# Performance work log

Measured on AMD Instinct MI355X. Metric: run time of the kernel, lower is better.

## Reference

```python
import jax, jax.numpy as jnp
import numpy as np

VOCAB, HID, KS, VS, EMB = 30, 512, 128, 128, 256
T, N, MAXLEN = 1000, 256, 250

def _lstm_cell(x, h, c, w_ih, w_hh, b_ih, b_hh):
    gates = x @ w_ih.T + h @ w_hh.T + b_ih + b_hh
    i, f, g, o = jnp.split(gates, 4, axis=-1)
    c2 = jax.nn.sigmoid(f) * c + jax.nn.sigmoid(i) * jnp.tanh(g)
    h2 = jax.nn.sigmoid(o) * jnp.tanh(c2)
    return h2, c2

def setup_inputs() -> dict:
    key = jax.random.key(0)
    ks = jax.random.split(key, 20)
    p = lambda k, shp: (jax.random.normal(k, shp, dtype=jnp.float32) * 0.05)
    inp = {
        'keys': jax.random.normal(ks[0], (T, N, KS), dtype=jnp.float32),
        'values': jax.random.normal(ks[1], (T, N, VS), dtype=jnp.float32),
        'seq_lengths': jax.random.randint(ks[2], (N,), 1, T + 1),
        'text': jax.random.randint(ks[3], (N, MAXLEN), 0, VOCAB),
        'embed_W': p(ks[4], (VOCAB, EMB)),
        'w_ih1': p(ks[5], (4 * HID, EMB + VS)), 'w_hh1': p(ks[6], (4 * HID, HID)),
        'b_ih1': jnp.zeros((4 * HID,), jnp.float32), 'b_hh1': jnp.zeros((4 * HID,), jnp.float32),
        'w_ih2': p(ks[7], (4 * HID, HID)), 'w_hh2': p(ks[8], (4 * HID, HID)),
        'b_ih2': jnp.zeros((4 * HID,), jnp.float32), 'b_hh2': jnp.zeros((4 * HID,), jnp.float32),
        'w_ih3': p(ks[9], (4 * KS, HID)), 'w_hh3': p(ks[10], (4 * KS, KS)),
        'b_ih3': jnp.zeros((4 * KS,), jnp.float32), 'b_hh3': jnp.zeros((4 * KS,), jnp.float32),
        'lin_W': p(ks[11], (KS, KS + VS)), 'lin_b': jnp.zeros((KS,), jnp.float32),
        'char_W': p(ks[12], (VOCAB, KS)), 'char_b': jnp.zeros((VOCAB,), jnp.float32),
    }
    return inp

def reference(keys, values, seq_lengths, text, embed_W,
              w_ih1, w_hh1, b_ih1, b_hh1,
              w_ih2, w_hh2, b_ih2, b_hh2,
              w_ih3, w_hh3, b_ih3, b_hh3,
              lin_W, lin_b, char_W, char_b):
    # teacher forcing path (deterministic), dropout is identity in reference
    mask = jnp.arange(T)[None, :] >= seq_lengths[:, None]          # (N, T)
    embs = embed_W[text]                                           # (N, MAXLEN, EMB)
    embs = jnp.swapaxes(embs, 0, 1)                                # (MAXLEN, N, EMB)

    def step(carry, emb_t):
        h1, c1, h2, c2, h3, c3, ctx = carry
        inp1 = jnp.concatenate([emb_t, ctx], axis=1)
        h1, c1 = _lstm_cell(inp1, h1, c1, w_ih1, w_hh1, b_ih1, b_hh1)
        h2, c2 = _lstm_cell(h1, h2, c2, w_ih2, w_hh2, b_ih2, b_hh2)
        h3, c3 = _lstm_cell(h2, h3, c3, w_ih3, w_hh3, b_ih3, b_hh3)
        energy = jnp.einsum('tnk,nk->nt', keys, h3)                # (N, T)
        energy = jnp.where(mask, -1e9, energy)
        attn = jax.nn.softmax(energy, axis=1)
        ctx2 = jnp.einsum('nt,tnv->nv', attn, values)              # (N, VS)
        pred = jnp.concatenate([h3, ctx2], axis=1) @ lin_W.T + lin_b
        pred = pred @ char_W.T + char_b                            # (N, VOCAB)
        return (h1, c1, h2, c2, h3, c3, ctx2), (pred, attn)

    z = lambda d: jnp.zeros((N, d), jnp.float32)
    init = (z(HID), z(HID), z(HID), z(HID), z(KS), z(KS), values[-1])
    _, (preds, attns) = jax.lax.scan(step, init, embs)
    return jnp.swapaxes(preds, 0, 1), attns                        # (N, MAXLEN, VOCAB), (MAXLEN, N, T)
```

## Files before the change

### kernel.cpp

```cpp
#include <hip/hip_runtime.h>

#define VOCAB  30
#define HID    512
#define KS     128
#define VS     128
#define EMB    256
#define TT     1000
#define NB     256
#define MAXLEN 250

#define NH (NB*HID)
#define NK (NB*KS)
#define OFF_CTX (6*NH + 3*NK)
#define WS_TOTAL (OFF_CTX + NK)
#define STATE_BYTES ((size_t)WS_TOTAL * 4)
#define VBF_BYTES   ((size_t)TT * NB * VS * 2)

#define K1 (EMB + VS + HID)
#define K2 (HID + HID)
#define K3 (HID + KS)
#define W1SZ (4*HID*K1)
#define W2SZ (4*HID*K2)
#define W3SZ (4*KS*K3)
#define EMBSZ (VOCAB*EMB)
#define BS1 (4*HID)
#define BS2 (4*HID)
#define BS3 (4*KS)

constexpr size_t NEW_BASE  = STATE_BYTES + VBF_BYTES;
constexpr size_t OFF_W1HI  = NEW_BASE;
constexpr size_t OFF_W1LO  = OFF_W1HI + (size_t)W1SZ*2;
constexpr size_t OFF_W2HI  = OFF_W1LO + (size_t)W1SZ*2;
constexpr size_t OFF_W2LO  = OFF_W2HI + (size_t)W2SZ*2;
constexpr size_t OFF_W3HI  = OFF_W2LO + (size_t)W2SZ*2;
constexpr size_t OFF_W3LO  = OFF_W3HI + (size_t)W3SZ*2;
constexpr size_t OFF_EMBHI = OFF_W3LO + (size_t)W3SZ*2;
constexpr size_t OFF_EMBLO = OFF_EMBHI + (size_t)EMBSZ*2;
constexpr size_t OFF_BSUM  = OFF_EMBLO + (size_t)EMBSZ*2;
constexpr size_t OFF_CTXHI = OFF_BSUM  + (size_t)(BS1+BS2+BS3)*4;
constexpr size_t OFF_CTXLO = OFF_CTXHI + (size_t)NB*VS*2;
constexpr size_t OFF_H1HI  = OFF_CTXLO + (size_t)NB*VS*2;
constexpr size_t OFF_H1LO  = OFF_H1HI + (size_t)2*NH*2;
constexpr size_t OFF_H2HI  = OFF_H1LO + (size_t)2*NH*2;
constexpr size_t OFF_H2LO  = OFF_H2HI + (size_t)2*NH*2;
constexpr size_t OFF_H3HI  = OFF_H2LO + (size_t)2*NH*2;
constexpr size_t OFF_H3LO  = OFF_H3HI + (size_t)2*NK*2;
constexpr size_t OFF_H3F   = OFF_H3LO + (size_t)2*NK*2;
constexpr size_t OFF_C1    = OFF_H3F  + (size_t)NK*4;
constexpr size_t OFF_C2    = OFF_C1 + (size_t)NH*4;
constexpr size_t OFF_C3    = OFF_C2 + (size_t)NH*4;
constexpr size_t FULL_BYTES= OFF_C3 + (size_t)NK*4;
constexpr size_t ZERO_BASE = OFF_H1HI;
constexpr size_t ZERO_BYTES= FULL_BYTES - OFF_H1HI;

typedef __attribute__((ext_vector_type(8))) short bf16x8;
typedef __attribute__((ext_vector_type(4))) float f32x4;
typedef unsigned short u16;

__device__ __forceinline__ float sigmoidf_(float x){ return 1.0f/(1.0f+__expf(-x)); }

__device__ __forceinline__ u16 f2bf_(float x){
    unsigned int u = __float_as_uint(x);
    return (u16)((u + 0x7fffu + ((u >> 16) & 1u)) >> 16);
}
__device__ __forceinline__ float bf2f_(u16 h){ return __uint_as_float((unsigned)h << 16); }


__global__ __launch_bounds__(256)
void pack_w_kernel(const float* __restrict__ wih, const float* __restrict__ whh,
                   u16* __restrict__ hi, u16* __restrict__ lo, int KIN, int KH, int total)
{
    int i = blockIdx.x*256 + threadIdx.x;
    if (i >= total) return;
    const int KW = KIN + KH;
    int g = i / KW, k = i - g*KW;
    float v = (k < KIN) ? wih[g*KIN + k] : whh[g*KH + (k - KIN)];
    u16 h = f2bf_(v);
    hi[i] = h;
    lo[i] = f2bf_(v - bf2f_(h));
}

__global__ __launch_bounds__(256)
void prep_misc_kernel(char* __restrict__ wsb, const float* __restrict__ embW,
                      const float* __restrict__ bi1, const float* __restrict__ bh1,
                      const float* __restrict__ bi2, const float* __restrict__ bh2,
                      const float* __restrict__ bi3, const float* __restrict__ bh3,
                      const float* __restrict__ values)
{
    const int gt = blockIdx.x*256 + threadIdx.x;
    const int gs = gridDim.x*256;
    u16* Ehi = (u16*)(wsb + OFF_EMBHI);
    u16* Elo = (u16*)(wsb + OFF_EMBLO);
    for (int i = gt; i < EMBSZ; i += gs){
        float v = embW[i]; u16 h = f2bf_(v);
        Ehi[i]=h; Elo[i]=f2bf_(v - bf2f_(h));
    }
    float* bs = (float*)(wsb + OFF_BSUM);
    for (int i = gt; i < BS1; i += gs) bs[i]         = bi1[i]+bh1[i];
    for (int i = gt; i < BS2; i += gs) bs[BS1+i]     = bi2[i]+bh2[i];
    for (int i = gt; i < BS3; i += gs) bs[BS1+BS2+i] = bi3[i]+bh3[i];
    u16* Chi = (u16*)(wsb + OFF_CTXHI);
    u16* Clo = (u16*)(wsb + OFF_CTXLO);
    const float* v0 = values + (size_t)(TT-1)*NB*VS;
    for (int i = gt; i < NB*VS; i += gs){
        float v = v0[i]; u16 h = f2bf_(v);
        Chi[i]=h; Clo[i]=f2bf_(v - bf2f_(h));
    }
    uint4* z = (uint4*)(wsb + ZERO_BASE);
    uint4 zz; zz.x=0; zz.y=0; zz.z=0; zz.w=0;
    for (size_t i = (size_t)gt; i < ZERO_BYTES/16; i += (size_t)gs) z[i] = zz;
}


__device__ __forceinline__ void lstm_step(const u16* const wh[4], const u16* const wl[4], int kw,
                                          bf16x8 ah, bf16x8 al, f32x4 acc[4])
{
    #pragma unroll
    for (int q=0;q<4;q++){
        bf16x8 wH = *(const bf16x8*)(wh[q] + kw);
        bf16x8 wL = *(const bf16x8*)(wl[q] + kw);
        acc[q] = __builtin_amdgcn_mfma_f32_16x16x32_bf16(ah, wH, acc[q], 0,0,0);
        acc[q] = __builtin_amdgcn_mfma_f32_16x16x32_bf16(al, wH, acc[q], 0,0,0);
        acc[q] = __builtin_amdgcn_mfma_f32_16x16x32_bf16(ah, wL, acc[q], 0,0,0);
    }
}

template<int H, int KIN, int KH, int MODE>
__global__ __launch_bounds__(256)
void lstm_mfma4(const u16* __restrict__ Whi, const u16* __restrict__ Wlo,
                const float* __restrict__ bsum,
                const u16* __restrict__ xhi, const u16* __restrict__ xlo,
                const u16* __restrict__ ehi, const u16* __restrict__ elo,
                const int* __restrict__ text, int step,
                const u16* __restrict__ hphi, const u16* __restrict__ hplo,
                u16* __restrict__ hohi, u16* __restrict__ holo,
                float* __restrict__ hof,
                float* __restrict__ cbuf)
{
    constexpr int KW  = KIN + KH;
    constexpr int HT  = H/16;
    constexpr int NT  = NB/16;
    constexpr int S32 = KW/32;
    constexpr int SPW = S32/4;
    static_assert(SPW*4 == S32, "K must split 4 ways");
    static_assert((HT & 7) == 0 || HT == 8, "HT divisible by 8");

    __shared__ float red[3][4][4][64];

    const int tid  = threadIdx.x;
    const int lane = tid & 63;
    const int wave = tid >> 6;

    const int bid = blockIdx.x;
    const int x = bid & 7, j = bid >> 3;
    const int ht = x*(HT/8) + j/NT;
    const int nt = j % NT;

    const int l15  = lane & 15, lhi = lane >> 4;
    const int n    = nt*16 + l15;
    const int koff = lhi*8;
    const int h0   = ht*16;

    const u16* wh[4]; const u16* wl[4];
    #pragma unroll
    for (int q=0;q<4;q++){
        size_t off = (size_t)(q*H + h0 + l15)*KW + koff;
        wh[q] = Whi + off; wl[q] = Wlo + off;
    }

    f32x4 acc[4];
    f32x4 zr = {0.f,0.f,0.f,0.f};
    #pragma unroll
    for (int q=0;q<4;q++) acc[q] = zr;

    const u16 *b0h, *b0l;
    if constexpr (MODE==0){
        const int trow = text[n*MAXLEN + step];
        b0h = ehi + trow*EMB + koff; b0l = elo + trow*EMB + koff;
    } else {
        b0h = xhi + n*KIN + koff;    b0l = xlo + n*KIN + koff;
    }
    const u16* bch = (MODE==0) ? (xhi + n*VS + koff) : nullptr;
    const u16* bcl = (MODE==0) ? (xlo + n*VS + koff) : nullptr;
    const u16* bhh = hphi + n*KH + koff;
    const u16* bhl = hplo + n*KH + koff;

    #pragma unroll
    for (int si=0; si<SPW; ++si){
        const int s = wave*SPW + si;
        const int k = s*32;
        const u16 *ph, *pl;
        if constexpr (MODE==0){
            if (k < EMB)          { ph = b0h + k;           pl = b0l + k; }
            else if (k < EMB+VS)  { ph = bch + (k-EMB);     pl = bcl + (k-EMB); }
            else                  { ph = bhh + (k-EMB-VS);  pl = bhl + (k-EMB-VS); }
        } else {
            if (k < KIN)          { ph = b0h + k;           pl = b0l + k; }
            else                  { ph = bhh + (k-KIN);     pl = bhl + (k-KIN); }
        }
        lstm_step(wh, wl, k, *(const bf16x8*)ph, *(const bf16x8*)pl, acc);
    }

    if (wave >= 1){
        #pragma unroll
        for (int q=0;q<4;q++)
            #pragma unroll
            for (int r=0;r<4;r++)
                red[wave-1][q][r][lane] = acc[q][r];
    }
    __syncthreads();

    if (wave == 0){
        #pragma unroll
        for (int q=0;q<4;q++)
            #pragma unroll
            for (int r=0;r<4;r++)
                acc[q][r] += red[0][q][r][lane] + red[1][q][r][lane] + red[2][q][r][lane];

        const int hcol = h0 + l15;
        const float bb0 = bsum[0*H + hcol], bb1 = bsum[1*H + hcol];
        const float bb2 = bsum[2*H + hcol], bb3 = bsum[3*H + hcol];
        const int nr0 = nt*16 + lhi*4;
        #pragma unroll
        for (int r=0;r<4;r++){
            const size_t p = (size_t)(nr0 + r)*H + hcol;
            const float gi = acc[0][r] + bb0;
            const float gf = acc[1][r] + bb1;
            const float gg = acc[2][r] + bb2;
            const float go = acc[3][r] + bb3;
            const float cn = sigmoidf_(gf)*cbuf[p] + sigmoidf_(gi)*tanhf(gg);
            const float hn = sigmoidf_(go)*tanhf(cn);
            cbuf[p] = cn;
            const u16 hb = f2bf_(hn);
            hohi[p] = hb;
            holo[p] = f2bf_(hn - bf2f_(hb));
            if (hof) hof[p] = hn;
        }
    }
}


__global__ __launch_bounds__(256)
void init_kernel(float* __restrict__ ws, const float* __restrict__ values){
    int i = blockIdx.x*256 + threadIdx.x;
    if (i >= WS_TOTAL) return;
    if (i < OFF_CTX) ws[i] = 0.0f;
    else ws[i] = values[(size_t)(TT-1)*NB*VS + (i - OFF_CTX)];
}

__global__ __launch_bounds__(256)
void conv_bf16_kernel(const float* __restrict__ src, u16* __restrict__ dst, int n4){
    int i = blockIdx.x*256 + threadIdx.x;
    if (i >= n4) return;
    float4 v = ((const float4*)src)[i];
    ushort4 o;
    o.x = f2bf_(v.x); o.y = f2bf_(v.y); o.z = f2bf_(v.z); o.w = f2bf_(v.w);
    ((ushort4*)dst)[i] = o;
}

template<int H, int KX, int KH, int MODE>
__global__ __launch_bounds__(256)
void lstm_kernel(const float* __restrict__ Wx, const float* __restrict__ Wh,
                 const float* __restrict__ bx, const float* __restrict__ bh,
                 const float* __restrict__ xbuf, const float* __restrict__ embW,
                 const int* __restrict__ text, int step,
                 const float* __restrict__ hread, float* __restrict__ hwrite,
                 float* __restrict__ cbuf)
{
    __shared__ __align__(16) float Xs[16][68];
    __shared__ __align__(16) float Ws[16][68];
    __shared__ float Gs[64][65];

    const int tid = threadIdx.x;
    const int h0  = blockIdx.x * 16;
    const int n0  = blockIdx.y * 64;

    const int sr = tid >> 2;
    const int sk = (tid & 3) << 2;
    const int wrow = (sr >> 4) * H + h0 + (sr & 15);
    const int n  = n0 + sr;

    const int tn4 = (tid & 15) * 4;
    const int tc4 = (tid >> 4) * 4;

    float acc[4][4];
    #pragma unroll
    for (int i=0;i<4;i++){
        #pragma unroll
        for (int j=0;j<4;j++) acc[i][j]=0.0f;
    }

    for (int k0 = 0; k0 < KX + KH; k0 += 16) {
        const int kb = k0 + sk;
        float4 xv, wv;
        if (k0 < KX) {
            if constexpr (MODE == 0) {
                if (kb < EMB) {
                    int idx = text[n * MAXLEN + step];
                    xv = *(const float4*)(embW + idx*EMB + kb);
                } else {
                    xv = *(const float4*)(xbuf + n*VS + (kb - EMB));
                }
            } else {
                xv = *(const float4*)(xbuf + n*KX + kb);
            }
            wv = *(const float4*)(Wx + wrow*KX + kb);
        } else {
            const int kh = kb - KX;
            xv = *(const float4*)(hread + n*KH + kh);
            wv = *(const float4*)(Wh + wrow*KH + kh);
        }
        Xs[sk+0][sr]=xv.x; Xs[sk+1][sr]=xv.y; Xs[sk+2][sr]=xv.z; Xs[sk+3][sr]=xv.w;
        Ws[sk+0][sr]=wv.x; Ws[sk+1][sr]=wv.y; Ws[sk+2][sr]=wv.z; Ws[sk+3][sr]=wv.w;
        __syncthreads();
        #pragma unroll
        for (int kk=0;kk<16;kk++){
            float4 xr = *(const float4*)&Xs[kk][tn4];
            float4 wr = *(const float4*)&Ws[kk][tc4];
            acc[0][0] += wr.x*xr.x; acc[0][1] += wr.x*xr.y; acc[0][2] += wr.x*xr.z; acc[0][3] += wr.x*xr.w;
            acc[1][0] += wr.y*xr.x; acc[1][1] += wr.y*xr.y; acc[1][2] += wr.y*xr.z; acc[1][3] += wr.y*xr.w;
            acc[2][0] += wr.z*xr.x; acc[2][1] += wr.z*xr.y; acc[2][2] += wr.z*xr.z; acc[2][3] += wr.z*xr.w;
            acc[3][0] += wr.w*xr.x; acc[3][1] += wr.w*xr.y; acc[3][2] += wr.w*xr.z; acc[3][3] += wr.w*xr.w;
        }
        __syncthreads();
    }

    #pragma unroll
    for (int ci=0; ci<4; ci++){
        const int c = tc4 + ci;
        const int row = (c >> 4) * H + h0 + (c & 15);
        const float b = bx[row] + bh[row];
        #pragma unroll
        for (int ni=0; ni<4; ni++) Gs[c][tn4+ni] = acc[ci][ni] + b;
    }
    __syncthreads();

    for (int p = tid; p < 16*64; p += 256){
        const int hl = p & 15, nl = p >> 4;
        const float gi = Gs[     hl][nl];
        const float gf = Gs[16 + hl][nl];
        const float gg = Gs[32 + hl][nl];
        const float go = Gs[48 + hl][nl];
        const int gn = n0 + nl, gh = h0 + hl;
        const float cold = cbuf[gn*H + gh];
        const float cn = sigmoidf_(gf)*cold + sigmoidf_(gi)*tanhf(gg);
        const float hn = sigmoidf_(go)*tanhf(cn);
        cbuf[gn*H + gh] = cn;
        hwrite[gn*H + gh] = hn;
    }
}

template<int BF, int CSPLIT>
__global__ __launch_bounds__(512)
void attn_pred_kernel(const float* __restrict__ keys, const void* __restrict__ values_v,
                      const int* __restrict__ seqlen, const float* __restrict__ h3,
                      const float* __restrict__ linW, const float* __restrict__ linb,
                      const float* __restrict__ charW, const float* __restrict__ charb,
                      float* __restrict__ ctx, u16* __restrict__ ctx_hi, u16* __restrict__ ctx_lo,
                      float* __restrict__ out, int step)
{
    __shared__ float es[TT];
    __shared__ float redm[8], reds[8];
    __shared__ float cpart[8][128];
    __shared__ float cat[256];
    __shared__ float mid[128];

    const int tid  = threadIdx.x;
    const int n    = blockIdx.x;
    const int wave = tid >> 6, lane = tid & 63;

    const float2 hv = *(const float2*)(h3 + n*KS + lane*2);
    const int L = seqlen[n];

    for (int t0 = wave*4; t0 < TT; t0 += 32) {
        const float2* kp = (const float2*)(keys + ((size_t)t0*NB + n)*KS) + lane;
        const size_t rs = (size_t)NB*KS/2;
        float2 k0 = kp[0], k1 = kp[rs], k2 = kp[2*rs], k3 = kp[3*rs];
        float d0 = k0.x*hv.x + k0.y*hv.y;
        float d1 = k1.x*hv.x + k1.y*hv.y;
        float d2 = k2.x*hv.x + k2.y*hv.y;
        float d3 = k3.x*hv.x + k3.y*hv.y;
        #pragma unroll
        for (int off=32; off; off>>=1){
            d0 += __shfl_xor(d0, off, 64);
            d1 += __shfl_xor(d1, off, 64);
            d2 += __shfl_xor(d2, off, 64);
            d3 += __shfl_xor(d3, off, 64);
        }
        if (lane == 0){
            es[t0+0] = (t0+0 < L) ? d0 : -1e9f;
            es[t0+1] = (t0+1 < L) ? d1 : -1e9f;
            es[t0+2] = (t0+2 < L) ? d2 : -1e9f;
            es[t0+3] = (t0+3 < L) ? d3 : -1e9f;
        }
    }
    __syncthreads();

    float m = -3e38f;
    for (int t = tid; t < TT; t += 512) m = fmaxf(m, es[t]);
    #pragma unroll
    for (int off=32; off; off>>=1) m = fmaxf(m, __shfl_xor(m, off, 64));
    if (lane == 0) redm[wave] = m;
    __syncthreads();
    m = redm[0];
    #pragma unroll
    for (int w=1; w<8; ++w) m = fmaxf(m, redm[w]);

    float s = 0.0f;
    for (int t = tid; t < TT; t += 512) { float p = __expf(es[t]-m); es[t] = p; s += p; }
    #pragma unroll
    for (int off=32; off; off>>=1) s += __shfl_xor(s, off, 64);
    if (lane == 0) reds[wave] = s;
    __syncthreads();
    s = reds[0];
    #pragma unroll
    for (int w=1; w<8; ++w) s += reds[w];
    const float inv = 1.0f / s;

    float* attn_out = out + (size_t)NB*MAXLEN*VOCAB + ((size_t)step*NB + n)*TT;
    for (int t = tid; t < TT; t += 512) { float a = es[t]*inv; es[t] = a; attn_out[t] = a; }
    __syncthreads();

    float cax = 0.0f, cay = 0.0f;
    if constexpr (BF) {
        const u16* vals = (const u16*)values_v;
        #pragma unroll 4
        for (int j = 0; j < 125; ++j){
            const int t = wave + 8*j;
            const float a = es[t];
            const unsigned int v2 = *((const unsigned int*)(vals + ((size_t)t*NB + n)*VS) + lane);
            cax += a * __uint_as_float(v2 << 16);
            cay += a * __uint_as_float(v2 & 0xffff0000u);
        }
    } else {
        const float* vals = (const float*)values_v;
        #pragma unroll 4
        for (int j = 0; j < 125; ++j){
            const int t = wave + 8*j;
            const float a = es[t];
            const float2 v2 = *((const float2*)(vals + ((size_t)t*NB + n)*VS) + lane);
            cax += a * v2.x;
            cay += a * v2.y;
        }
    }
    cpart[wave][lane*2]   = cax;
    cpart[wave][lane*2+1] = cay;
    __syncthreads();

    if (tid < 128) {
        float cv = 0.0f;
        #pragma unroll
        for (int w=0; w<8; ++w) cv += cpart[w][tid];
        if constexpr (CSPLIT) {
            const u16 hb = f2bf_(cv);
            ctx_hi[n*VS + tid] = hb;
            ctx_lo[n*VS + tid] = f2bf_(cv - bf2f_(hb));
        } else {
            ctx[n*VS + tid] = cv;
        }
        cat[tid]        = h3[n*KS + tid];
        cat[128 + tid]  = cv;
    }
    __syncthreads();

    if (tid < 256) {
        const int o  = tid >> 1;
        const int kh = (tid & 1) * 128;
        const float* w = linW + o*(KS+VS) + kh;
        float a = 0.0f;
        #pragma unroll 8
        for (int k=0; k<128; ++k) a += w[k]*cat[kh+k];
        a += __shfl_xor(a, 1, 64);
        if (!(tid & 1)) mid[o] = a + linb[o];
    }
    __syncthreads();

    if (tid < VOCAB) {
        float a = charb[tid];
        const float* w = charW + tid*KS;
        #pragma unroll 8
        for (int k=0; k<KS; ++k) a += w[k]*mid[k];
        out[((size_t)n*MAXLEN + step)*VOCAB + tid] = a;
    }
}


extern "C" void kernel_launch(void* const* d_in, const int* in_sizes, int n_in,
                              void* d_out, int out_size, void* d_ws, size_t ws_size,
                              hipStream_t stream)
{
    const float* keys   = (const float*)d_in[0];
    const float* values = (const float*)d_in[1];
    const int*   seqlen = (const int*)  d_in[2];
    const int*   text   = (const int*)  d_in[3];
    const float* embW   = (const float*)d_in[4];
    const float* w_ih1  = (const float*)d_in[5];
    const float* w_hh1  = (const float*)d_in[6];
    const float* b_ih1  = (const float*)d_in[7];
    const float* b_hh1  = (const float*)d_in[8];
    const float* w_ih2  = (const float*)d_in[9];
    const float* w_hh2  = (const float*)d_in[10];
    const float* b_ih2  = (const float*)d_in[11];
    const float* b_hh2  = (const float*)d_in[12];
    const float* w_ih3  = (const float*)d_in[13];
    const float* w_hh3  = (const float*)d_in[14];
    const float* b_ih3  = (const float*)d_in[15];
    const float* b_hh3  = (const float*)d_in[16];
    const float* linW   = (const float*)d_in[17];
    const float* linb   = (const float*)d_in[18];
    const float* charW  = (const float*)d_in[19];
    const float* charb  = (const float*)d_in[20];
    float* out = (float*)d_out;
    float* ws  = (float*)d_ws;
    char*  wsb = (char*)d_ws;

    u16* vals_bf = (u16*)(wsb + STATE_BYTES);
    const int n4 = TT*NB*VS/4;

    if (ws_size >= FULL_BYTES) {
        u16* W1hi=(u16*)(wsb+OFF_W1HI); u16* W1lo=(u16*)(wsb+OFF_W1LO);
        u16* W2hi=(u16*)(wsb+OFF_W2HI); u16* W2lo=(u16*)(wsb+OFF_W2LO);
        u16* W3hi=(u16*)(wsb+OFF_W3HI); u16* W3lo=(u16*)(wsb+OFF_W3LO);
        u16* Ehi =(u16*)(wsb+OFF_EMBHI); u16* Elo =(u16*)(wsb+OFF_EMBLO);
        float* bs=(float*)(wsb+OFF_BSUM);
        u16* Chi =(u16*)(wsb+OFF_CTXHI); u16* Clo =(u16*)(wsb+OFF_CTXLO);
        u16* H1hi=(u16*)(wsb+OFF_H1HI);  u16* H1lo=(u16*)(wsb+OFF_H1LO);
        u16* H2hi=(u16*)(wsb+OFF_H2HI);  u16* H2lo=(u16*)(wsb+OFF_H2LO);
        u16* H3hi=(u16*)(wsb+OFF_H3HI);  u16* H3lo=(u16*)(wsb+OFF_H3LO);
        float* H3f=(float*)(wsb+OFF_H3F);
        float* C1=(float*)(wsb+OFF_C1);
        float* C2=(float*)(wsb+OFF_C2);
        float* C3=(float*)(wsb+OFF_C3);

        pack_w_kernel<<<(W1SZ+255)/256, 256, 0, stream>>>(w_ih1, w_hh1, W1hi, W1lo, EMB+VS, HID, W1SZ);
        pack_w_kernel<<<(W2SZ+255)/256, 256, 0, stream>>>(w_ih2, w_hh2, W2hi, W2lo, HID,    HID, W2SZ);
        pack_w_kernel<<<(W3SZ+255)/256, 256, 0, stream>>>(w_ih3, w_hh3, W3hi, W3lo, HID,    KS,  W3SZ);
        conv_bf16_kernel<<<(n4 + 255)/256, 256, 0, stream>>>(values, vals_bf, n4);
        prep_misc_kernel<<<1024, 256, 0, stream>>>(wsb, embW, b_ih1,b_hh1, b_ih2,b_hh2, b_ih3,b_hh3, values);

        constexpr int G12 = (HID/16)*(NB/16);
        constexpr int G3  = (KS/16)*(NB/16);

        for (int t = 0; t < MAXLEN; ++t) {
            const int cur = t & 1, nxt = cur ^ 1;
            lstm_mfma4<HID, EMB+VS, HID, 0><<<G12, 256, 0, stream>>>(
                W1hi, W1lo, bs, Chi, Clo, Ehi, Elo, text, t,
                H1hi + cur*NH, H1lo + cur*NH,
                H1hi + nxt*NH, H1lo + nxt*NH, nullptr, C1);
            lstm_mfma4<HID, HID, HID, 1><<<G12, 256, 0, stream>>>(
                W2hi, W2lo, bs + BS1, H1hi + nxt*NH, H1lo + nxt*NH, nullptr, nullptr, nullptr, 0,
                H2hi + cur*NH, H2lo + cur*NH,
                H2hi + nxt*NH, H2lo + nxt*NH, nullptr, C2);
            lstm_mfma4<KS, HID, KS, 1><<<G3, 256, 0, stream>>>(
                W3hi, W3lo, bs + BS1 + BS2, H2hi + nxt*NH, H2lo + nxt*NH, nullptr, nullptr, nullptr, 0,
                H3hi + cur*NK, H3lo + cur*NK,
                H3hi + nxt*NK, H3lo + nxt*NK, H3f, C3);
            attn_pred_kernel<1,1><<<NB, 512, 0, stream>>>(
                keys, vals_bf, seqlen, H3f, linW, linb, charW, charb,
                nullptr, Chi, Clo, out, t);
        }
        return;
    }

    float* h1  = ws;
    float* c1  = h1 + 2*NH;
    float* h2  = c1 + NH;
    float* c2  = h2 + 2*NH;
    float* h3  = c2 + NH;
    float* c3  = h3 + 2*NK;
    float* ctx = c3 + NK;

    const bool use_bf16 = (ws_size >= STATE_BYTES + VBF_BYTES);

    init_kernel<<<(WS_TOTAL + 255)/256, 256, 0, stream>>>(ws, values);
    if (use_bf16) {
        conv_bf16_kernel<<<(n4 + 255)/256, 256, 0, stream>>>(values, vals_bf, n4);
    }

    for (int t = 0; t < MAXLEN; ++t) {
        const int cur = t & 1, nxt = cur ^ 1;
        lstm_kernel<HID, EMB+VS, HID, 0><<<dim3(HID/16, NB/64), 256, 0, stream>>>(
            w_ih1, w_hh1, b_ih1, b_hh1, ctx, embW, text, t,
            h1 + cur*NH, h1 + nxt*NH, c1);
        lstm_kernel<HID, HID, HID, 1><<<dim3(HID/16, NB/64), 256, 0, stream>>>(
            w_ih2, w_hh2, b_ih2, b_hh2, h1 + nxt*NH, nullptr, nullptr, t,
            h2 + cur*NH, h2 + nxt*NH, c2);
        lstm_kernel<KS, HID, KS, 1><<<dim3(KS/16, NB/64), 256, 0, stream>>>(
            w_ih3, w_hh3, b_ih3, b_hh3, h2 + nxt*NH, nullptr, nullptr, t,
            h3 + cur*NK, h3 + nxt*NK, c3);
        if (use_bf16)
            attn_pred_kernel<1,0><<<NB, 512, 0, stream>>>(
                keys, vals_bf, seqlen, h3 + nxt*NK,
                linW, linb, charW, charb, ctx, nullptr, nullptr, out, t);
        else
            attn_pred_kernel<0,0><<<NB, 512, 0, stream>>>(
                keys, values, seqlen, h3 + nxt*NK,
                linW, linb, charW, charb, ctx, nullptr, nullptr, out, t);
    }
}
```

Baseline: 27.76 ms.

## Use fp16 keys/values in attention, skip masked keys, tile LSTM over two batch tiles

Keys and values are converted once to fp16 in workspace, so the attention kernel reads half the bytes per step, and key loads for timesteps past the sequence length are skipped. The layer-1/2 LSTM kernels now process two 16-row batch tiles per block, reusing each weight load across both tiles and halving the grid. The reduction now spreads across waves and tiles. This risks some fp16 precision loss in attention and requires a larger workspace, falling back to bf16 if the workspace is too small.

```diff
diff --git a/kernel.cpp b/kernel.cpp
--- a/kernel.cpp
+++ b/kernel.cpp
@@ -1,4 +1,5 @@
 #include <hip/hip_runtime.h>
+#include <hip/hip_fp16.h>
 
 #define VOCAB  30
 #define HID    512
@@ -53,6 +54,10 @@
 constexpr size_t ZERO_BASE = OFF_H1HI;
 constexpr size_t ZERO_BYTES= FULL_BYTES - OFF_H1HI;
 
+constexpr size_t OFF_KF16   = FULL_BYTES;
+constexpr size_t KF16_BYTES = (size_t)TT*NB*KS*2;
+constexpr size_t FULL2_BYTES= OFF_KF16 + KF16_BYTES;
+
 typedef __attribute__((ext_vector_type(8))) short bf16x8;
 typedef __attribute__((ext_vector_type(4))) float f32x4;
 typedef unsigned short u16;
@@ -111,21 +116,31 @@
     for (size_t i = (size_t)gt; i < ZERO_BYTES/16; i += (size_t)gs) z[i] = zz;
 }
 
-
-__device__ __forceinline__ void lstm_step(const u16* const wh[4], const u16* const wl[4], int kw,
-                                          bf16x8 ah, bf16x8 al, f32x4 acc[4])
-{
-    #pragma unroll
-    for (int q=0;q<4;q++){
-        bf16x8 wH = *(const bf16x8*)(wh[q] + kw);
-        bf16x8 wL = *(const bf16x8*)(wl[q] + kw);
-        acc[q] = __builtin_amdgcn_mfma_f32_16x16x32_bf16(ah, wH, acc[q], 0,0,0);
-        acc[q] = __builtin_amdgcn_mfma_f32_16x16x32_bf16(al, wH, acc[q], 0,0,0);
-        acc[q] = __builtin_amdgcn_mfma_f32_16x16x32_bf16(ah, wL, acc[q], 0,0,0);
-    }
-}
-
-template<int H, int KIN, int KH, int MODE>
+__global__ __launch_bounds__(256)
+void conv_bf16_kernel(const float* __restrict__ src, u16* __restrict__ dst, int n4){
+    int i = blockIdx.x*256 + threadIdx.x;
+    if (i >= n4) return;
+    float4 v = ((const float4*)src)[i];
+    ushort4 o;
+    o.x = f2bf_(v.x); o.y = f2bf_(v.y); o.z = f2bf_(v.z); o.w = f2bf_(v.w);
+    ((ushort4*)dst)[i] = o;
+}
+
+__global__ __launch_bounds__(256)
+void conv_f16_kernel(const float* __restrict__ src, u16* __restrict__ dst, int n4){
+    int i = blockIdx.x*256 + threadIdx.x;
+    if (i >= n4) return;
+    float4 v = ((const float4*)src)[i];
+    ushort4 o;
+    o.x = __half_as_ushort(__float2half(v.x));
+    o.y = __half_as_ushort(__float2half(v.y));
+    o.z = __half_as_ushort(__float2half(v.z));
+    o.w = __half_as_ushort(__float2half(v.w));
+    ((ushort4*)dst)[i] = o;
+}
+
+
+template<int H, int KIN, int KH, int MODE, int NTILE>
 __global__ __launch_bounds__(256)
 void lstm_mfma4(const u16* __restrict__ Whi, const u16* __restrict__ Wlo,
                 const float* __restrict__ bsum,
@@ -140,12 +155,13 @@
     constexpr int KW  = KIN + KH;
     constexpr int HT  = H/16;
     constexpr int NT  = NB/16;
+    constexpr int NTP = NT/NTILE;
     constexpr int S32 = KW/32;
     constexpr int SPW = S32/4;
     static_assert(SPW*4 == S32, "K must split 4 ways");
-    static_assert((HT & 7) == 0 || HT == 8, "HT divisible by 8");
-
-    __shared__ float red[3][4][4][64];
+    static_assert(NT % NTILE == 0, "NTILE divides NT");
+
+    __shared__ float red[4][NTILE][4][4][64];
 
     const int tid  = threadIdx.x;
     const int lane = tid & 63;
@@ -153,11 +169,10 @@
 
     const int bid = blockIdx.x;
     const int x = bid & 7, j = bid >> 3;
-    const int ht = x*(HT/8) + j/NT;
-    const int nt = j % NT;
+    const int ht  = x*(HT/8) + j/NTP;
+    const int ntp = j % NTP;
 
     const int l15  = lane & 15, lhi = lane >> 4;
-    const int n    = nt*16 + l15;
     const int koff = lhi*8;
     const int h0   = ht*16;
 
@@ -168,66 +183,91 @@
         wh[q] = Whi + off; wl[q] = Wlo + off;
     }
 
-    f32x4 acc[4];
+    f32x4 acc[NTILE][4];
     f32x4 zr = {0.f,0.f,0.f,0.f};
     #pragma unroll
-    for (int q=0;q<4;q++) acc[q] = zr;
-
-    const u16 *b0h, *b0l;
-    if constexpr (MODE==0){
-        const int trow = text[n*MAXLEN + step];
-        b0h = ehi + trow*EMB + koff; b0l = elo + trow*EMB + koff;
-    } else {
-        b0h = xhi + n*KIN + koff;    b0l = xlo + n*KIN + koff;
-    }
-    const u16* bch = (MODE==0) ? (xhi + n*VS + koff) : nullptr;
-    const u16* bcl = (MODE==0) ? (xlo + n*VS + koff) : nullptr;
-    const u16* bhh = hphi + n*KH + koff;
-    const u16* bhl = hplo + n*KH + koff;
+    for (int f=0;f<NTILE;f++)
+        #pragma unroll
+        for (int q=0;q<4;q++) acc[f][q] = zr;
+
+    const u16 *b0h[NTILE], *b0l[NTILE], *bch[NTILE], *bcl[NTILE], *bhh[NTILE], *bhl[NTILE];
+    #pragma unroll
+    for (int f=0;f<NTILE;f++){
+        const int n = (ntp*NTILE + f)*16 + l15;
+        if constexpr (MODE==0){
+            const int trow = text[n*MAXLEN + step];
+            b0h[f] = ehi + trow*EMB + koff; b0l[f] = elo + trow*EMB + koff;
+            bch[f] = xhi + n*VS + koff;     bcl[f] = xlo + n*VS + koff;
+        } else {
+            b0h[f] = xhi + n*KIN + koff;    b0l[f] = xlo + n*KIN + koff;
+            bch[f] = nullptr;               bcl[f] = nullptr;
+        }
+        bhh[f] = hphi + n*KH + koff;
+        bhl[f] = hplo + n*KH + koff;
+    }
 
     #pragma unroll
     for (int si=0; si<SPW; ++si){
         const int s = wave*SPW + si;
         const int k = s*32;
-        const u16 *ph, *pl;
-        if constexpr (MODE==0){
-            if (k < EMB)          { ph = b0h + k;           pl = b0l + k; }
-            else if (k < EMB+VS)  { ph = bch + (k-EMB);     pl = bcl + (k-EMB); }
-            else                  { ph = bhh + (k-EMB-VS);  pl = bhl + (k-EMB-VS); }
-        } else {
-            if (k < KIN)          { ph = b0h + k;           pl = b0l + k; }
-            else                  { ph = bhh + (k-KIN);     pl = bhl + (k-KIN); }
-        }
-        lstm_step(wh, wl, k, *(const bf16x8*)ph, *(const bf16x8*)pl, acc);
-    }
-
-    if (wave >= 1){
+        bf16x8 ah[NTILE], al[NTILE];
+        #pragma unroll
+        for (int f=0;f<NTILE;f++){
+            const u16 *ph, *pl;
+            if constexpr (MODE==0){
+                if (k < EMB)          { ph = b0h[f] + k;          pl = b0l[f] + k; }
+                else if (k < EMB+VS)  { ph = bch[f] + (k-EMB);    pl = bcl[f] + (k-EMB); }
+                else                  { ph = bhh[f] + (k-EMB-VS); pl = bhl[f] + (k-EMB-VS); }
+            } else {
+                if (k < KIN)          { ph = b0h[f] + k;          pl = b0l[f] + k; }
+                else                  { ph = bhh[f] + (k-KIN);    pl = bhl[f] + (k-KIN); }
+            }
+            ah[f] = *(const bf16x8*)ph;
+            al[f] = *(const bf16x8*)pl;
+        }
+        #pragma unroll
+        for (int q=0;q<4;q++){
+            bf16x8 wH = *(const bf16x8*)(wh[q] + k);
+            bf16x8 wL = *(const bf16x8*)(wl[q] + k);
+            #pragma unroll
+            for (int f=0;f<NTILE;f++){
+                acc[f][q] = __builtin_amdgcn_mfma_f32_16x16x32_bf16(ah[f], wH, acc[f][q], 0,0,0);
+                acc[f][q] = __builtin_amdgcn_mfma_f32_16x16x32_bf16(al[f], wH, acc[f][q], 0,0,0);
+                acc[f][q] = __builtin_amdgcn_mfma_f32_16x16x32_bf16(ah[f], wL, acc[f][q], 0,0,0);
+            }
+        }
+    }
+
+    #pragma unroll
+    for (int f=0;f<NTILE;f++)
         #pragma unroll
         for (int q=0;q<4;q++)
             #pragma unroll
             for (int r=0;r<4;r++)
-                red[wave-1][q][r][lane] = acc[q][r];
-    }
-    __syncthreads();
-
-    if (wave == 0){
+                red[wave][f][q][r][lane] = acc[f][q][r];
+    __syncthreads();
+
+    if (wave < NTILE){
+        const int f = wave;
+        float a4[4][4];
         #pragma unroll
         for (int q=0;q<4;q++)
             #pragma unroll
             for (int r=0;r<4;r++)
-                acc[q][r] += red[0][q][r][lane] + red[1][q][r][lane] + red[2][q][r][lane];
+                a4[q][r] = red[0][f][q][r][lane] + red[1][f][q][r][lane]
+                         + red[2][f][q][r][lane] + red[3][f][q][r][lane];
 
         const int hcol = h0 + l15;
         const float bb0 = bsum[0*H + hcol], bb1 = bsum[1*H + hcol];
         const float bb2 = bsum[2*H + hcol], bb3 = bsum[3*H + hcol];
-        const int nr0 = nt*16 + lhi*4;
+        const int nr0 = (ntp*NTILE + f)*16 + lhi*4;
         #pragma unroll
         for (int r=0;r<4;r++){
             const size_t p = (size_t)(nr0 + r)*H + hcol;
-            const float gi = acc[0][r] + bb0;
-            const float gf = acc[1][r] + bb1;
-            const float gg = acc[2][r] + bb2;
-            const float go = acc[3][r] + bb3;
+            const float gi = a4[0][r] + bb0;
+            const float gf = a4[1][r] + bb1;
+            const float gg = a4[2][r] + bb2;
+            const float go = a4[3][r] + bb3;
             const float cn = sigmoidf_(gf)*cbuf[p] + sigmoidf_(gi)*tanhf(gg);
             const float hn = sigmoidf_(go)*tanhf(cn);
             cbuf[p] = cn;
@@ -246,16 +286,6 @@
     if (i >= WS_TOTAL) return;
     if (i < OFF_CTX) ws[i] = 0.0f;
     else ws[i] = values[(size_t)(TT-1)*NB*VS + (i - OFF_CTX)];
-}
-
-__global__ __launch_bounds__(256)
-void conv_bf16_kernel(const float* __restrict__ src, u16* __restrict__ dst, int n4){
-    int i = blockIdx.x*256 + threadIdx.x;
-    if (i >= n4) return;
-    float4 v = ((const float4*)src)[i];
-    ushort4 o;
-    o.x = f2bf_(v.x); o.y = f2bf_(v.y); o.z = f2bf_(v.z); o.w = f2bf_(v.w);
-    ((ushort4*)dst)[i] = o;
 }
 
 template<int H, int KX, int KH, int MODE>
@@ -352,7 +382,8 @@
 
 template<int BF, int CSPLIT>
 __global__ __launch_bounds__(512)
-void attn_pred_kernel(const float* __restrict__ keys, const void* __restrict__ values_v,
+void attn_pred_kernel(const float* __restrict__ keys, const u16* __restrict__ keysF,
+                      const void* __restrict__ values_v,
                       const int* __restrict__ seqlen, const float* __restrict__ h3,
                       const float* __restrict__ linW, const float* __restrict__ linb,
                       const float* __restrict__ charW, const float* __restrict__ charb,
@@ -372,26 +403,60 @@
     const float2 hv = *(const float2*)(h3 + n*KS + lane*2);
     const int L = seqlen[n];
 
-    for (int t0 = wave*4; t0 < TT; t0 += 32) {
-        const float2* kp = (const float2*)(keys + ((size_t)t0*NB + n)*KS) + lane;
-        const size_t rs = (size_t)NB*KS/2;
-        float2 k0 = kp[0], k1 = kp[rs], k2 = kp[2*rs], k3 = kp[3*rs];
-        float d0 = k0.x*hv.x + k0.y*hv.y;
-        float d1 = k1.x*hv.x + k1.y*hv.y;
-        float d2 = k2.x*hv.x + k2.y*hv.y;
-        float d3 = k3.x*hv.x + k3.y*hv.y;
-        #pragma unroll
-        for (int off=32; off; off>>=1){
-            d0 += __shfl_xor(d0, off, 64);
-            d1 += __shfl_xor(d1, off, 64);
-            d2 += __shfl_xor(d2, off, 64);
-            d3 += __shfl_xor(d3, off, 64);
-        }
-        if (lane == 0){
-            es[t0+0] = (t0+0 < L) ? d0 : -1e9f;
-            es[t0+1] = (t0+1 < L) ? d1 : -1e9f;
-            es[t0+2] = (t0+2 < L) ? d2 : -1e9f;
-            es[t0+3] = (t0+3 < L) ? d3 : -1e9f;
+    if constexpr (BF == 2) {
+        for (int t0 = wave*4; t0 < TT; t0 += 32) {
+            if (t0 >= L) {
+                if (lane == 0){
+                    es[t0+0] = -1e9f; es[t0+1] = -1e9f; es[t0+2] = -1e9f; es[t0+3] = -1e9f;
+                }
+                continue;
+            }
+            const __half2* kp = (const __half2*)(keysF + ((size_t)t0*NB + n)*KS) + lane;
+            const size_t rs = (size_t)NB*KS/2;
+            float2 k0 = __half22float2(kp[0]);
+            float2 k1 = __half22float2(kp[rs]);
+            float2 k2 = __half22float2(kp[2*rs]);
+            float2 k3 = __half22float2(kp[3*rs]);
+            float d0 = k0.x*hv.x + k0.y*hv.y;
+            float d1 = k1.x*hv.x + k1.y*hv.y;
+            float d2 = k2.x*hv.x + k2.y*hv.y;
+            float d3 = k3.x*hv.x + k3.y*hv.y;
+            #pragma unroll
+            for (int off=32; off; off>>=1){
+                d0 += __shfl_xor(d0, off, 64);
+                d1 += __shfl_xor(d1, off, 64);
+                d2 += __shfl_xor(d2, off, 64);
+                d3 += __shfl_xor(d3, off, 64);
+            }
+            if (lane == 0){
+                es[t0+0] = (t0+0 < L) ? d0 : -1e9f;
+                es[t0+1] = (t0+1 < L) ? d1 : -1e9f;
+                es[t0+2] = (t0+2 < L) ? d2 : -1e9f;
+                es[t0+3] = (t0+3 < L) ? d3 : -1e9f;
+            }
+        }
+    } else {
+        for (int t0 = wave*4; t0 < TT; t0 += 32) {
+            const float2* kp = (const float2*)(keys + ((size_t)t0*NB + n)*KS) + lane;
+            const size_t rs = (size_t)NB*KS/2;
+            float2 k0 = kp[0], k1 = kp[rs], k2 = kp[2*rs], k3 = kp[3*rs];
+            float d0 = k0.x*hv.x + k0.y*hv.y;
+            float d1 = k1.x*hv.x + k1.y*hv.y;
+            float d2 = k2.x*hv.x + k2.y*hv.y;
+            float d3 = k3.x*hv.x + k3.y*hv.y;
+            #pragma unroll
+            for (int off=32; off; off>>=1){
+                d0 += __shfl_xor(d0, off, 64);
+                d1 += __shfl_xor(d1, off, 64);
+                d2 += __shfl_xor(d2, off, 64);
+                d3 += __shfl_xor(d3, off, 64);
+            }
+            if (lane == 0){
+                es[t0+0] = (t0+0 < L) ? d0 : -1e9f;
+                es[t0+1] = (t0+1 < L) ? d1 : -1e9f;
+                es[t0+2] = (t0+2 < L) ? d2 : -1e9f;
+                es[t0+3] = (t0+3 < L) ? d3 : -1e9f;
+            }
         }
     }
     __syncthreads();
@@ -422,7 +487,18 @@
     __syncthreads();
 
     float cax = 0.0f, cay = 0.0f;
-    if constexpr (BF) {
+    if constexpr (BF == 2) {
+        const u16* vals = (const u16*)values_v;
+        for (int j = 0; j < 125; ++j){
+            const int t = wave + 8*j;
+            if (t >= L) break;
+            const float a = es[t];
+            __half2 v2 = *((const __half2*)(vals + ((size_t)t*NB + n)*VS) + lane);
+            float2 vf = __half22float2(v2);
+            cax += a * vf.x;
+            cay += a * vf.y;
+        }
+    } else if constexpr (BF == 1) {
         const u16* vals = (const u16*)values_v;
         #pragma unroll 4
         for (int j = 0; j < 125; ++j){
@@ -514,10 +590,13 @@
     float* ws  = (float*)d_ws;
     char*  wsb = (char*)d_ws;
 
-    u16* vals_bf = (u16*)(wsb + STATE_BYTES);
-    const int n4 = TT*NB*VS/4;
+    u16* vals16 = (u16*)(wsb + STATE_BYTES);
+    const int n4v = TT*NB*VS/4;
+    const int n4k = TT*NB*KS/4;
 
     if (ws_size >= FULL_BYTES) {
+        const bool f16 = (ws_size >= FULL2_BYTES);
+
         u16* W1hi=(u16*)(wsb+OFF_W1HI); u16* W1lo=(u16*)(wsb+OFF_W1LO);
         u16* W2hi=(u16*)(wsb+OFF_W2HI); u16* W2lo=(u16*)(wsb+OFF_W2LO);
         u16* W3hi=(u16*)(wsb+OFF_W3HI); u16* W3lo=(u16*)(wsb+OFF_W3LO);
@@ -531,33 +610,44 @@
         float* C1=(float*)(wsb+OFF_C1);
         float* C2=(float*)(wsb+OFF_C2);
         float* C3=(float*)(wsb+OFF_C3);
+        u16* keysF=(u16*)(wsb+OFF_KF16);
 
         pack_w_kernel<<<(W1SZ+255)/256, 256, 0, stream>>>(w_ih1, w_hh1, W1hi, W1lo, EMB+VS, HID, W1SZ);
         pack_w_kernel<<<(W2SZ+255)/256, 256, 0, stream>>>(w_ih2, w_hh2, W2hi, W2lo, HID,    HID, W2SZ);
         pack_w_kernel<<<(W3SZ+255)/256, 256, 0, stream>>>(w_ih3, w_hh3, W3hi, W3lo, HID,    KS,  W3SZ);
-        conv_bf16_kernel<<<(n4 + 255)/256, 256, 0, stream>>>(values, vals_bf, n4);
+        if (f16) {
+            conv_f16_kernel<<<(n4v + 255)/256, 256, 0, stream>>>(values, vals16, n4v);
+            conv_f16_kernel<<<(n4k + 255)/256, 256, 0, stream>>>(keys,   keysF,  n4k);
+        } else {
+            conv_bf16_kernel<<<(n4v + 255)/256, 256, 0, stream>>>(values, vals16, n4v);
+        }
         prep_misc_kernel<<<1024, 256, 0, stream>>>(wsb, embW, b_ih1,b_hh1, b_ih2,b_hh2, b_ih3,b_hh3, values);
 
-        constexpr int G12 = (HID/16)*(NB/16);
+        constexpr int G12 = (HID/16)*(NB/16)/2;
         constexpr int G3  = (KS/16)*(NB/16);
 
         for (int t = 0; t < MAXLEN; ++t) {
             const int cur = t & 1, nxt = cur ^ 1;
-            lstm_mfma4<HID, EMB+VS, HID, 0><<<G12, 256, 0, stream>>>(
+            lstm_mfma4<HID, EMB+VS, HID, 0, 2><<<G12, 256, 0, stream>>>(
                 W1hi, W1lo, bs, Chi, Clo, Ehi, Elo, text, t,
                 H1hi + cur*NH, H1lo + cur*NH,
                 H1hi + nxt*NH, H1lo + nxt*NH, nullptr, C1);
-            lstm_mfma4<HID, HID, HID, 1><<<G12, 256, 0, stream>>>(
+            lstm_mfma4<HID, HID, HID, 1, 2><<<G12, 256, 0, stream>>>(
                 W2hi, W2lo, bs + BS1, H1hi + nxt*NH, H1lo + nxt*NH, nullptr, nullptr, nullptr, 0,
                 H2hi + cur*NH, H2lo + cur*NH,
                 H2hi + nxt*NH, H2lo + nxt*NH, nullptr, C2);
-            lstm_mfma4<KS, HID, KS, 1><<<G3, 256, 0, stream>>>(
+            lstm_mfma4<KS, HID, KS, 1, 1><<<G3, 256, 0, stream>>>(
                 W3hi, W3lo, bs + BS1 + BS2, H2hi + nxt*NH, H2lo + nxt*NH, nullptr, nullptr, nullptr, 0,
                 H3hi + cur*NK, H3lo + cur*NK,
                 H3hi + nxt*NK, H3lo + nxt*NK, H3f, C3);
-            attn_pred_kernel<1,1><<<NB, 512, 0, stream>>>(
-                keys, vals_bf, seqlen, H3f, linW, linb, charW, charb,
-                nullptr, Chi, Clo, out, t);
+            if (f16)
+                attn_pred_kernel<2,1><<<NB, 512, 0, stream>>>(
+                    keys, keysF, vals16, seqlen, H3f, linW, linb, charW, charb,
+                    nullptr, Chi, Clo, out, t);
+            else
+                attn_pred_kernel<1,1><<<NB, 512, 0, stream>>>(
+                    keys, nullptr, vals16, seqlen, H3f, linW, linb, charW, charb,
+                    nullptr, Chi, Clo, out, t);
         }
         return;
     }
@@ -574,7 +664,7 @@
 
     init_kernel<<<(WS_TOTAL + 255)/256, 256, 0, stream>>>(ws, values);
     if (use_bf16) {
-        conv_bf16_kernel<<<(n4 + 255)/256, 256, 0, stream>>>(values, vals_bf, n4);
+        conv_bf16_kernel<<<(n4v + 255)/256, 256, 0, stream>>>(values, vals16, n4v);
     }
 
     for (int t = 0; t < MAXLEN; ++t) {
@@ -590,11 +680,11 @@
             h3 + cur*NK, h3 + nxt*NK, c3);
         if (use_bf16)
             attn_pred_kernel<1,0><<<NB, 512, 0, stream>>>(
-                keys, vals_bf, seqlen, h3 + nxt*NK,
+                keys, nullptr, vals16, seqlen, h3 + nxt*NK,
                 linW, linb, charW, charb, ctx, nullptr, nullptr, out, t);
         else
             attn_pred_kernel<0,0><<<NB, 512, 0, stream>>>(
-                keys, values, seqlen, h3 + nxt*NK,
+                keys, nullptr, values, seqlen, h3 + nxt*NK,
                 linW, linb, charW, charb, ctx, nullptr, nullptr, out, t);
     }
 }
```

Result: slower. 29.80 ms (+7.3%).
